# Kernel optimization log

Measured on AMD Instinct MI355X. Metric: run time of the kernel, lower is better.

Reference implementation:

```python
import jax, jax.numpy as jnp
import numpy as np

B, T, D, H, E, K, F = 8, 1024, 512, 8, 8, 2, 2048
HD = D // H
EPS = 1e-5


def _layernorm(x, g, b):
    m = jnp.mean(x, axis=-1, keepdims=True)
    v = jnp.mean((x - m) ** 2, axis=-1, keepdims=True)
    return (x - m) * jax.lax.rsqrt(v + EPS) * g + b


def setup_inputs() -> dict:
    key = jax.random.key(0)
    ks = jax.random.split(key, 12)
    s = lambda d: 1.0 / np.sqrt(d)
    return {
        "x": jax.random.normal(ks[0], (B, T, D), jnp.float32),
        "ln1_g": jnp.ones((D,), jnp.float32),
        "ln1_b": jnp.zeros((D,), jnp.float32),
        "ln2_g": jnp.ones((D,), jnp.float32),
        "ln2_b": jnp.zeros((D,), jnp.float32),
        "Wqkv": jax.random.normal(ks[1], (D, 3 * D), jnp.float32) * s(D),
        "bqkv": jnp.zeros((3 * D,), jnp.float32),
        "Wo": jax.random.normal(ks[2], (D, D), jnp.float32) * s(D),
        "bo": jnp.zeros((D,), jnp.float32),
        "Wg": jax.random.normal(ks[3], (D, E), jnp.float32) * s(D),
        "We1": jax.random.normal(ks[4], (E, D, F), jnp.float32) * s(D),
        "be1": jnp.zeros((E, F), jnp.float32),
        "We2": jax.random.normal(ks[5], (E, F, D), jnp.float32) * s(F),
        "be2": jnp.zeros((E, D), jnp.float32),
    }


def _attn(x, Wqkv, bqkv, Wo, bo):
    qkv = x @ Wqkv + bqkv                      # [B,T,3D]
    q, k, v = jnp.split(qkv, 3, axis=-1)
    q = q.reshape(B, T, H, HD)
    k = k.reshape(B, T, H, HD)
    v = v.reshape(B, T, H, HD)
    scores = jnp.einsum("bqhd,bkhd->bhqk", q, k) / np.sqrt(HD)
    causal = jnp.tril(jnp.ones((T, T), bool))
    scores = jnp.where(causal, scores, jnp.finfo(scores.dtype).min)
    p = jax.nn.softmax(scores, axis=-1)
    o = jnp.einsum("bhqk,bkhd->bqhd", p, v).reshape(B, T, D)
    return o @ Wo + bo


def _moe(h, Wg, We1, be1, We2, be2):
    hf = h.reshape(-1, D)                      # [N,D]
    N = hf.shape[0]
    probs = jax.nn.softmax(hf @ Wg, axis=-1)   # [N,E]
    topw, topi = jax.lax.top_k(probs, K)       # [N,K]
    topw = topw / jnp.sum(topw, axis=-1, keepdims=True)
    gates = jnp.zeros((N, E), hf.dtype).at[jnp.arange(N)[:, None], topi].add(topw)
    out = jnp.zeros_like(hf)
    for e in range(E):                         # fixed small expert loop
        hid = jax.nn.gelu(hf @ We1[e] + be1[e])
        out = out + gates[:, e:e + 1] * (hid @ We2[e] + be2[e])
    return out.reshape(h.shape)


def reference(x, ln1_g, ln1_b, ln2_g, ln2_b, Wqkv, bqkv, Wo, bo, Wg, We1, be1, We2, be2):
    # Pipeline chunking over batch is a scheduling detail; math is the plain block.
    h = x + _attn(_layernorm(x, ln1_g, ln1_b), Wqkv, bqkv, Wo, bo)
    return h + _moe(_layernorm(h, ln2_g, ln2_b), Wg, We1, be1, We2, be2)
```

## Files before the change

### kernel.cpp

```cpp
#include <hip/hip_runtime.h>


typedef unsigned short u16;
typedef unsigned int   u32;
typedef unsigned long long u64;
typedef __attribute__((ext_vector_type(8))) short short8;
typedef __attribute__((ext_vector_type(4))) float f32x4;

#define DEV static __device__ __forceinline__

DEV u16 f2bf(float f){
  union { float f; u32 u; } x; x.f = f;
  return (u16)((x.u + 0x7FFFu + ((x.u >> 16) & 1u)) >> 16);
}
DEV float bf2f(u16 b){
  union { u32 u; float f; } x; x.u = ((u32)b) << 16; return x.f;
}
DEV f32x4 mfma16(short8 a, short8 b, f32x4 c){
  return __builtin_amdgcn_mfma_f32_16x16x32_bf16(a, b, c, 0, 0, 0);
}
DEV void g2l16(const void* g, void* l){
  __builtin_amdgcn_global_load_lds((const __attribute__((address_space(1))) u32*)g,
                                   (__attribute__((address_space(3))) u32*)l, 16, 0, 0);
}
DEV void wait_vm0(){ asm volatile("s_waitcnt vmcnt(0)" ::: "memory"); }

__global__ __launch_bounds__(256) void transpose_cvt2(const float* __restrict__ src,
    u16* __restrict__ dh, u16* __restrict__ dl, int R, int C)
{
  __shared__ float tile[32][33];
  const size_t zb = (size_t)blockIdx.z * R * C;
  src += zb; dh += zb; dl += zb;
  const int tx = threadIdx.x, ty = threadIdx.y;
  const int c0 = blockIdx.x * 32, r0 = blockIdx.y * 32;
  #pragma unroll
  for (int i = 0; i < 4; ++i)
    tile[ty + i*8][tx] = src[(size_t)(r0 + ty + i*8) * C + c0 + tx];
  __syncthreads();
  #pragma unroll
  for (int i = 0; i < 4; ++i){
    float v = tile[tx][ty + i*8];
    size_t o = (size_t)(c0 + ty + i*8) * R + r0 + tx;
    u16 hb = f2bf(v);
    dh[o] = hb;
    dl[o] = f2bf(v - bf2f(hb));
  }
}

__global__ __launch_bounds__(256) void transpose_cvt1(const float* __restrict__ src,
    u16* __restrict__ d, int R, int C)
{
  __shared__ float tile[32][33];
  const size_t zb = (size_t)blockIdx.z * R * C;
  src += zb; d += zb;
  const int tx = threadIdx.x, ty = threadIdx.y;
  const int c0 = blockIdx.x * 32, r0 = blockIdx.y * 32;
  #pragma unroll
  for (int i = 0; i < 4; ++i)
    tile[ty + i*8][tx] = src[(size_t)(r0 + ty + i*8) * C + c0 + tx];
  __syncthreads();
  #pragma unroll
  for (int i = 0; i < 4; ++i)
    d[(size_t)(c0 + ty + i*8) * R + r0 + tx] = f2bf(tile[tx][ty + i*8]);
}

__global__ __launch_bounds__(256) void ln1_kernel(const float* __restrict__ x,
    const float* __restrict__ g, const float* __restrict__ b,
    u16* __restrict__ yh, u16* __restrict__ yl)
{
  const int wid = threadIdx.x >> 6, lane = threadIdx.x & 63;
  const int row = blockIdx.x * 4 + wid;
  const float* xr = x + (size_t)row * 512 + lane * 8;
  f32x4 t0 = ((const f32x4*)xr)[0], t1 = ((const f32x4*)xr)[1];
  float v[8];
  #pragma unroll
  for (int j = 0; j < 8; ++j) v[j] = (j < 4) ? t0[j] : t1[j-4];
  float s = 0.f, q = 0.f;
  #pragma unroll
  for (int j = 0; j < 8; ++j){ s += v[j]; q += v[j]*v[j]; }
  #pragma unroll
  for (int o = 32; o; o >>= 1){ s += __shfl_xor(s, o); q += __shfl_xor(q, o); }
  const float mean = s * (1.f/512.f);
  const float var  = q * (1.f/512.f) - mean*mean;
  const float rstd = rsqrtf(var + 1e-5f);
  f32x4 g0 = ((const f32x4*)(g + lane*8))[0], g1 = ((const f32x4*)(g + lane*8))[1];
  f32x4 b0 = ((const f32x4*)(b + lane*8))[0], b1 = ((const f32x4*)(b + lane*8))[1];
  short8 vh, vl;
  #pragma unroll
  for (int j = 0; j < 8; ++j){
    float gg = (j < 4) ? g0[j] : g1[j-4];
    float bb = (j < 4) ? b0[j] : b1[j-4];
    float y = (v[j]-mean)*rstd*gg + bb;
    u16 hb = f2bf(y);
    vh[j] = (short)hb;
    vl[j] = (short)f2bf(y - bf2f(hb));
  }
  ((short8*)(yh + (size_t)row*512 + lane*8))[0] = vh;
  ((short8*)(yl + (size_t)row*512 + lane*8))[0] = vl;
}

template<int MODE>
__global__ __launch_bounds__(256) void gemm_split2(
    const u16* __restrict__ Ah, const u16* __restrict__ Al,
    const u16* __restrict__ Bh, const u16* __restrict__ Bl,
    const float* __restrict__ bias, int K,
    u16* __restrict__ q_h, u16* __restrict__ q_l, u16* __restrict__ q_m,
    u16* __restrict__ k_h, u16* __restrict__ k_l, u16* __restrict__ k_m,
    u16* __restrict__ v_h, u16* __restrict__ v_l,
    const float* __restrict__ xres, float* __restrict__ hout)
{
  __shared__ u16 Ash[2][128*32], Asl[2][128*32], Bsh[2][128*32], Bsl[2][128*32];
  const int tid = threadIdx.x;
  const int wid = tid >> 6, lane = tid & 63;
  const int wr = wid >> 1, wc = wid & 1;
  const int lr = lane & 15, lg = lane >> 4;
  const int m0 = blockIdx.x * 128, n0 = blockIdx.y * 128;

  size_t aoff[2], boff[2];
  u32 ldso[2];
  #pragma unroll
  for (int r = 0; r < 2; ++r){
    int i = r*256 + tid;
    int row = i >> 2, cc = i & 3;
    int scc = cc ^ ((row >> 1) & 3);
    aoff[r] = ((size_t)(m0+row)*K + scc*8) * 2;
    boff[r] = ((size_t)(n0+row)*K + scc*8) * 2;
    ldso[r] = (u32)(r*256 + wid*64) * 8;
  }

  f32x4 acc[4][4];
  #pragma unroll
  for (int a = 0; a < 4; ++a)
    #pragma unroll
    for (int b = 0; b < 4; ++b) acc[a][b] = 0;

  const char* pAh = (const char*)Ah; const char* pAl = (const char*)Al;
  const char* pBh = (const char*)Bh; const char* pBl = (const char*)Bl;

  auto stage = [&](int sb, int ks){
    const size_t kb = (size_t)ks * 64;
    #pragma unroll
    for (int r = 0; r < 2; ++r){
      g2l16(pAh + aoff[r] + kb, &Ash[sb][0] + ldso[r]);
      g2l16(pAl + aoff[r] + kb, &Asl[sb][0] + ldso[r]);
      g2l16(pBh + boff[r] + kb, &Bsh[sb][0] + ldso[r]);
      g2l16(pBl + boff[r] + kb, &Bsl[sb][0] + ldso[r]);
    }
  };

  const int nks = K >> 5;
  stage(0, 0);
  wait_vm0();
  __syncthreads();
  int buf = 0;
  for (int ks = 0; ks < nks; ++ks){
    if (ks + 1 < nks) stage(buf ^ 1, ks + 1);
    short8 ah[4], al[4], bh[4], bl[4];
    #pragma unroll
    for (int mt = 0; mt < 4; ++mt){
      int row = wr*64 + mt*16 + lr;
      int kcs = lg ^ ((row >> 1) & 3);
      int o = row*32 + kcs*8;
      ah[mt] = *(const short8*)(&Ash[buf][0] + o);
      al[mt] = *(const short8*)(&Asl[buf][0] + o);
    }
    #pragma unroll
    for (int nt = 0; nt < 4; ++nt){
      int row = wc*64 + nt*16 + lr;
      int kcs = lg ^ ((row >> 1) & 3);
      int o = row*32 + kcs*8;
      bh[nt] = *(const short8*)(&Bsh[buf][0] + o);
      bl[nt] = *(const short8*)(&Bsl[buf][0] + o);
    }
    __builtin_amdgcn_s_setprio(1);
    #pragma unroll
    for (int mt = 0; mt < 4; ++mt)
      #pragma unroll
      for (int nt = 0; nt < 4; ++nt){
        f32x4 c = acc[mt][nt];
        c = mfma16(ah[mt], bh[nt], c);
        c = mfma16(ah[mt], bl[nt], c);
        c = mfma16(al[mt], bh[nt], c);
        acc[mt][nt] = c;
      }
    __builtin_amdgcn_s_setprio(0);
    wait_vm0();
    __syncthreads();
    buf ^= 1;
  }

  #pragma unroll
  for (int mt = 0; mt < 4; ++mt){
    #pragma unroll
    for (int nt = 0; nt < 4; ++nt){
      const int col = n0 + wc*64 + nt*16 + lr;
      const float bv = bias[col];
      #pragma unroll
      for (int r2 = 0; r2 < 4; ++r2){
        const int row = m0 + wr*64 + mt*16 + 4*lg + r2;
        const float val = acc[mt][nt][r2] + bv;
        if constexpr (MODE == 0){
          const int which = col >> 9, rem = col & 511;
          const int hh = rem >> 6, hd = rem & 63;
          const int b_ = row >> 10, t_ = row & 1023;
          const size_t idx = ((size_t)(b_*8 + hh)*1024 + t_)*64 + hd;
          const u16 hb = f2bf(val);
          if (which == 2){
            v_h[idx] = hb;
            v_l[idx] = f2bf(val - bf2f(hb));
          } else {
            const float r1 = val - bf2f(hb);
            const u16 lb = f2bf(r1);
            const u16 mb = f2bf(r1 - bf2f(lb));
            if (which == 0){ q_h[idx]=hb; q_l[idx]=lb; q_m[idx]=mb; }
            else           { k_h[idx]=hb; k_l[idx]=lb; k_m[idx]=mb; }
          }
        } else {
          const size_t o = (size_t)row*512 + col;
          hout[o] = val + xres[o];
        }
      }
    }
  }
}

__global__ __launch_bounds__(256) void attn_kernel(
    const u16* __restrict__ q_h, const u16* __restrict__ q_l, const u16* __restrict__ q_m,
    const u16* __restrict__ k_h, const u16* __restrict__ k_l, const u16* __restrict__ k_m,
    const u16* __restrict__ v_h, const u16* __restrict__ v_l,
    u16* __restrict__ aoh, u16* __restrict__ aol)
{
  __shared__ u16 Ksh[64*64], Ksl[64*64], Ksm[64*64];
  __shared__ u16 Vth[64*72], Vtl[64*72];
  __shared__ u16 Ph[4*16*72], Pl[4*16*72];
  const int tid = threadIdx.x, wid = tid >> 6, lane = tid & 63;
  const int lr = lane & 15, lg = lane >> 4;
  const int bfl = blockIdx.x;
  const int xcd = bfl & 7, jj_ = bfl >> 3;
  const int bh = xcd * 8 + (jj_ & 7);
  const int qt = 15 - (jj_ >> 3);
  const int q0 = qt * 64;
  const size_t base = (size_t)bh * 1024 * 64;

  short8 qfh[2], qfl[2], qfm[2];
  {
    const int qrow = q0 + wid*16 + lr;
    #pragma unroll
    for (int c = 0; c < 2; ++c){
      const size_t o = base + (size_t)qrow*64 + c*32 + lg*8;
      qfh[c] = *(const short8*)(q_h + o);
      qfl[c] = *(const short8*)(q_l + o);
      qfm[c] = *(const short8*)(q_m + o);
    }
  }
  f32x4 oacc[4];
  float m_r[4], l_r[4];
  #pragma unroll
  for (int nt = 0; nt < 4; ++nt) oacc[nt] = 0;
  #pragma unroll
  for (int r = 0; r < 4; ++r){ m_r[r] = -1e30f; l_r[r] = 0.f; }

  short8 kreg[3][2];
  short8 vreg[2][2];
  const int pp = tid & 31, d0 = (tid >> 5) * 8;

  auto load_tile = [&](int kt){
    #pragma unroll
    for (int r = 0; r < 2; ++r){
      const int i = r*256 + tid;
      const int row = i >> 3, cc = i & 7;
      const int scc = cc ^ (row & 7);
      const size_t go = base + (size_t)(kt*64 + row)*64 + scc*8;
      kreg[0][r] = *(const short8*)(k_h + go);
      kreg[1][r] = *(const short8*)(k_l + go);
      kreg[2][r] = *(const short8*)(k_m + go);
    }
    const size_t g0 = base + (size_t)(kt*64 + 2*pp)*64 + d0;
    vreg[0][0] = *(const short8*)(v_h + g0);
    vreg[0][1] = *(const short8*)(v_h + g0 + 64);
    vreg[1][0] = *(const short8*)(v_l + g0);
    vreg[1][1] = *(const short8*)(v_l + g0 + 64);
  };

  load_tile(0);
  for (int kt = 0; kt <= qt; ++kt){
    if (kt) __syncthreads();
    #pragma unroll
    for (int r = 0; r < 2; ++r){
      const int o = (r*256 + tid) * 8;
      *(short8*)(Ksh + o) = kreg[0][r];
      *(short8*)(Ksl + o) = kreg[1][r];
      *(short8*)(Ksm + o) = kreg[2][r];
    }
    #pragma unroll
    for (int j = 0; j < 8; ++j){
      u32 ph_ = (u32)(u16)vreg[0][0][j] | ((u32)(u16)vreg[0][1][j] << 16);
      u32 pl_ = (u32)(u16)vreg[1][0][j] | ((u32)(u16)vreg[1][1][j] << 16);
      *(u32*)(Vth + (d0+j)*72 + 2*pp) = ph_;
      *(u32*)(Vtl + (d0+j)*72 + 2*pp) = pl_;
    }
    __syncthreads();
    if (kt < qt) load_tile(kt + 1);
    __builtin_amdgcn_sched_barrier(0);

    f32x4 s[4];
    #pragma unroll
    for (int nt = 0; nt < 4; ++nt) s[nt] = 0;
    __builtin_amdgcn_s_setprio(1);
    #pragma unroll
    for (int c = 0; c < 2; ++c){
      #pragma unroll
      for (int nt = 0; nt < 4; ++nt){
        const int row = nt*16 + lr;
        const int kcs = (c*4 + lg) ^ (row & 7);
        const int o = row*64 + kcs*8;
        short8 kh_ = *(const short8*)(Ksh + o);
        short8 kl_ = *(const short8*)(Ksl + o);
        short8 km_ = *(const short8*)(Ksm + o);
        f32x4 cacc = s[nt];
        cacc = mfma16(qfh[c], kh_, cacc);
        cacc = mfma16(qfh[c], kl_, cacc);
        cacc = mfma16(qfl[c], kh_, cacc);
        cacc = mfma16(qfh[c], km_, cacc);
        cacc = mfma16(qfm[c], kh_, cacc);
        cacc = mfma16(qfl[c], kl_, cacc);
        s[nt] = cacc;
      }
    }
    __builtin_amdgcn_s_setprio(0);
    float sc[4][4];
    const bool last = (kt == qt);
    #pragma unroll
    for (int nt = 0; nt < 4; ++nt)
      #pragma unroll
      for (int r = 0; r < 4; ++r){
        float v = s[nt][r] * 0.125f;
        if (last){
          int qa = q0 + wid*16 + 4*lg + r;
          int ka = kt*64 + nt*16 + lr;
          if (ka > qa) v = -1e30f;
        }
        sc[nt][r] = v;
      }
    float pr[4][4];
    #pragma unroll
    for (int r = 0; r < 4; ++r){
      float mx = fmaxf(fmaxf(sc[0][r], sc[1][r]), fmaxf(sc[2][r], sc[3][r]));
      #pragma unroll
      for (int o2 = 8; o2; o2 >>= 1) mx = fmaxf(mx, __shfl_xor(mx, o2));
      const float nm = fmaxf(m_r[r], mx);
      const float al = __expf(m_r[r] - nm);
      float sum = 0.f;
      #pragma unroll
      for (int nt = 0; nt < 4; ++nt){
        float e_ = __expf(sc[nt][r] - nm);
        pr[nt][r] = e_;
        sum += e_;
      }
      #pragma unroll
      for (int o2 = 8; o2; o2 >>= 1) sum += __shfl_xor(sum, o2);
      l_r[r] = l_r[r]*al + sum;
      m_r[r] = nm;
      #pragma unroll
      for (int nt = 0; nt < 4; ++nt) oacc[nt][r] *= al;
    }
    #pragma unroll
    for (int nt = 0; nt < 4; ++nt)
      #pragma unroll
      for (int r = 0; r < 4; ++r){
        const float pv = pr[nt][r];
        const u16 hb = f2bf(pv);
        const u16 lb = f2bf(pv - bf2f(hb));
        const int o = wid*1152 + (4*lg + r)*72 + nt*16 + lr;
        Ph[o] = hb; Pl[o] = lb;
      }
    #pragma unroll
    for (int c = 0; c < 2; ++c){
      const int po = wid*1152 + lr*72 + c*32 + lg*8;
      short8 pah = *(const short8*)(Ph + po);
      short8 pal = *(const short8*)(Pl + po);
      __builtin_amdgcn_s_setprio(1);
      #pragma unroll
      for (int nt = 0; nt < 4; ++nt){
        const int vo = (nt*16 + lr)*72 + c*32 + lg*8;
        short8 vhf = *(const short8*)(Vth + vo);
        short8 vlf = *(const short8*)(Vtl + vo);
        f32x4 cacc = oacc[nt];
        cacc = mfma16(pah, vhf, cacc);
        cacc = mfma16(pah, vlf, cacc);
        cacc = mfma16(pal, vhf, cacc);
        oacc[nt] = cacc;
      }
      __builtin_amdgcn_s_setprio(0);
    }
  }

  const int b_ = bh >> 3, h_ = bh & 7;
  #pragma unroll
  for (int nt = 0; nt < 4; ++nt)
    #pragma unroll
    for (int r = 0; r < 4; ++r){
      const int qa = q0 + wid*16 + 4*lg + r;
      const float val = oacc[nt][r] / l_r[r];
      const size_t o = ((size_t)(b_*1024 + qa))*512 + h_*64 + nt*16 + lr;
      const u16 hb = f2bf(val);
      aoh[o] = hb;
      aol[o] = f2bf(val - bf2f(hb));
    }
}

__global__ __launch_bounds__(256) void ln2_gate_kernel(const float* __restrict__ h,
    const float* __restrict__ g, const float* __restrict__ b,
    const float* __restrict__ Wg, u16* __restrict__ y2,
    int* __restrict__ ge, float* __restrict__ gw)
{
  const int wid = threadIdx.x >> 6, lane = threadIdx.x & 63;
  const int row = blockIdx.x * 4 + wid;
  const float* xr = h + (size_t)row * 512 + lane * 8;
  f32x4 t0 = ((const f32x4*)xr)[0], t1 = ((const f32x4*)xr)[1];
  float v[8];
  #pragma unroll
  for (int j = 0; j < 8; ++j) v[j] = (j < 4) ? t0[j] : t1[j-4];
  float s = 0.f, q = 0.f;
  #pragma unroll
  for (int j = 0; j < 8; ++j){ s += v[j]; q += v[j]*v[j]; }
  #pragma unroll
  for (int o = 32; o; o >>= 1){ s += __shfl_xor(s, o); q += __shfl_xor(q, o); }
  const float mean = s * (1.f/512.f);
  const float var  = q * (1.f/512.f) - mean*mean;
  const float rstd = rsqrtf(var + 1e-5f);
  f32x4 g0 = ((const f32x4*)(g + lane*8))[0], g1 = ((const f32x4*)(g + lane*8))[1];
  f32x4 b0 = ((const f32x4*)(b + lane*8))[0], b1 = ((const f32x4*)(b + lane*8))[1];
  float yv[8];
  short8 yb;
  #pragma unroll
  for (int j = 0; j < 8; ++j){
    float gg = (j < 4) ? g0[j] : g1[j-4];
    float bb = (j < 4) ? b0[j] : b1[j-4];
    yv[j] = (v[j]-mean)*rstd*gg + bb;
    yb[j] = (short)f2bf(yv[j]);
  }
  ((short8*)(y2 + (size_t)row*512 + lane*8))[0] = yb;

  float lgt[8];
  #pragma unroll
  for (int e = 0; e < 8; ++e) lgt[e] = 0.f;
  #pragma unroll
  for (int j = 0; j < 8; ++j){
    const float* wr_ = Wg + (size_t)(lane*8 + j) * 8;
    #pragma unroll
    for (int e = 0; e < 8; ++e) lgt[e] += yv[j] * wr_[e];
  }
  #pragma unroll
  for (int o = 32; o; o >>= 1){
    #pragma unroll
    for (int e = 0; e < 8; ++e) lgt[e] += __shfl_xor(lgt[e], o);
  }
  if (lane == 0){
    int e0 = 0; float l0 = lgt[0];
    #pragma unroll
    for (int e = 1; e < 8; ++e) if (lgt[e] > l0){ l0 = lgt[e]; e0 = e; }
    int e1 = -1; float l1 = -3e38f;
    #pragma unroll
    for (int e = 0; e < 8; ++e) if (e != e0 && lgt[e] > l1){ l1 = lgt[e]; e1 = e; }
    const float t = expf(l1 - l0);
    const float w0 = 1.f / (1.f + t);
    const float w1 = t * w0;
    ge[row*2]   = e0; ge[row*2+1] = e1;
    gw[row*2]   = w0; gw[row*2+1] = w1;
  }
}

__global__ __launch_bounds__(256) void count_kernel(const int* __restrict__ ge,
                                                    int* __restrict__ cnt)
{
  const int i = blockIdx.x * 256 + threadIdx.x;
  const int lane = threadIdx.x & 63;
  const int e = ge[i];
  #pragma unroll
  for (int ex = 0; ex < 8; ++ex){
    u64 m = __ballot(e == ex);
    if (m && lane == (int)(__ffsll((long long)m) - 1))
      atomicAdd(&cnt[ex], __popcll(m));
  }
}

__global__ void offsets_kernel(int* cnt){
  if (threadIdx.x == 0){
    int o = 0, tp = 0;
    for (int e = 0; e < 8; ++e){
      cnt[8+e] = o; cnt[17+e] = o;
      cnt[25+e] = tp;
      o  += cnt[e];
      tp += (cnt[e] + 127) >> 7;
    }
    cnt[16] = o;
    cnt[33] = tp;
  }
}

__global__ __launch_bounds__(256) void scatter_kernel(const int* __restrict__ ge,
    const float* __restrict__ gw, int* __restrict__ cnt,
    int* __restrict__ rdst, float* __restrict__ rw)
{
  const int i = blockIdx.x * 256 + threadIdx.x;
  const int lane = threadIdx.x & 63;
  const int e = ge[i];
  const float w = gw[i];
  const u64 below = ((u64)1 << lane) - 1;
  int pos = -1;
  #pragma unroll
  for (int ex = 0; ex < 8; ++ex){
    u64 m = __ballot(e == ex);
    if (m){
      const int leader = (int)(__ffsll((long long)m) - 1);
      int base = 0;
      if (lane == leader) base = atomicAdd(&cnt[17 + ex], __popcll(m));
      base = __shfl(base, leader);
      if (e == ex) pos = base + __popcll(m & below);
    }
  }
  rdst[pos] = i;
  rw[pos]   = w;
}

template<int MODE, int TN>
__global__ __launch_bounds__(256, 4) void gemm_moe(
    const u16* __restrict__ A, const u16* __restrict__ Bt,
    const float* __restrict__ bias, int N, int K,
    const int* __restrict__ cntblk,
    const int* __restrict__ rdst, const float* __restrict__ rw,
    u16* __restrict__ hid, float* __restrict__ contrib)
{
  __shared__ u16 As[2][128*32], Bs[2][128*32];
  const int fid = blockIdx.x;
  const int xcd = fid & 7;
  const int j   = fid >> 3;
  const int bpb = 2 * TN;
  const int bi  = j / bpb;
  const int band = bi * 8 + xcd;
  const int r_  = j % bpb;
  const int nt_ = r_ / 2;
  const int mi  = r_ % 2;
  const int mt  = band * 2 + mi;
  if (mt >= cntblk[33]) return;
  int e = 7;
  #pragma unroll
  for (int k = 7; k >= 1; --k) if (mt < cntblk[25 + k]) e = k - 1;
  const int ce = cntblk[e];
  const int eo = cntblk[8 + e];
  const int m0 = (mt - cntblk[25 + e]) * 128;
  const int n0 = nt_ * 128;

  const int tid = threadIdx.x;
  const int wid = tid >> 6, lane = tid & 63;
  const int wr = wid >> 1, wc = wid & 1;
  const int lr = lane & 15, lg = lane >> 4;

  size_t aoff[2], boff[2];
  u32 ldso[2];
  #pragma unroll
  for (int r = 0; r < 2; ++r){
    int i = r*256 + tid;
    int row = i >> 2, cc = i & 3;
    int scc = cc ^ ((row >> 1) & 3);
    int p = eo + m0 + row;
    const int pmax = eo + ce - 1;
    if (p > pmax) p = pmax;
    const int arow = (MODE == 2) ? (rdst[p] >> 1) : p;
    aoff[r] = ((size_t)arow * K + scc*8) * 2;
    boff[r] = (((size_t)e * N + n0 + row) * K + scc*8) * 2;
    ldso[r] = (u32)(r*256 + wid*64) * 8;
  }

  f32x4 acc[4][4];
  #pragma unroll
  for (int a = 0; a < 4; ++a)
    #pragma unroll
    for (int b = 0; b < 4; ++b) acc[a][b] = 0;

  const char* pA = (const char*)A;
  const char* pB = (const char*)Bt;

  auto stage = [&](int sb, int ks){
    const size_t kb = (size_t)ks * 64;
    #pragma unroll
    for (int r = 0; r < 2; ++r){
      g2l16(pA + aoff[r] + kb, &As[sb][0] + ldso[r]);
      g2l16(pB + boff[r] + kb, &Bs[sb][0] + ldso[r]);
    }
  };

  const int nks = K >> 5;
  stage(0, 0);
  wait_vm0();
  __syncthreads();
  int buf = 0;
  for (int ks = 0; ks < nks; ++ks){
    if (ks + 1 < nks) stage(buf ^ 1, ks + 1);
    short8 av[4], bv[4];
    #pragma unroll
    for (int mt2 = 0; mt2 < 4; ++mt2){
      int row = wr*64 + mt2*16 + lr;
      int kcs = lg ^ ((row >> 1) & 3);
      av[mt2] = *(const short8*)(&As[buf][0] + row*32 + kcs*8);
    }
    #pragma unroll
    for (int nt2 = 0; nt2 < 4; ++nt2){
      int row = wc*64 + nt2*16 + lr;
      int kcs = lg ^ ((row >> 1) & 3);
      bv[nt2] = *(const short8*)(&Bs[buf][0] + row*32 + kcs*8);
    }
    __builtin_amdgcn_s_setprio(1);
    #pragma unroll
    for (int mt2 = 0; mt2 < 4; ++mt2)
      #pragma unroll
      for (int nt2 = 0; nt2 < 4; ++nt2)
        acc[mt2][nt2] = mfma16(av[mt2], bv[nt2], acc[mt2][nt2]);
    __builtin_amdgcn_s_setprio(0);
    wait_vm0();
    __syncthreads();
    buf ^= 1;
  }

  const float* bp = bias + (size_t)e * N;
  #pragma unroll
  for (int mt2 = 0; mt2 < 4; ++mt2){
    #pragma unroll
    for (int nt2 = 0; nt2 < 4; ++nt2){
      const int col = n0 + wc*64 + nt2*16 + lr;
      const float bv2 = bp[col];
      #pragma unroll
      for (int r2 = 0; r2 < 4; ++r2){
        const int lrow = wr*64 + mt2*16 + 4*lg + r2;
        if (m0 + lrow < ce){
          const int p = eo + m0 + lrow;
          const float val = acc[mt2][nt2][r2] + bv2;
          if constexpr (MODE == 2){
            const float gx = val;
            const float z2 = 1.5957691216057308f * (gx + 0.044715f*gx*gx*gx);
            const float gl = gx / (1.f + __expf(-z2));
            hid[(size_t)p * N + col] = f2bf(gl);
          } else {
            contrib[(size_t)rdst[p] * 512 + col] = val * rw[p];
          }
        }
      }
    }
  }
}

__global__ __launch_bounds__(256) void final_kernel(const float* __restrict__ h,
    const float* __restrict__ contrib, float* __restrict__ out)
{
  const int i = blockIdx.x * 256 + threadIdx.x;
  const int row = i >> 7, rem = i & 127;
  const f32x4* c4 = (const f32x4*)contrib;
  f32x4 hv = ((const f32x4*)h)[i];
  const size_t b2 = (size_t)(row * 2) * 128 + rem;
  f32x4 a0 = c4[b2];
  f32x4 a1 = c4[b2 + 128];
  ((f32x4*)out)[i] = hv + a0 + a1;
}

extern "C" void kernel_launch(void* const* d_in, const int* in_sizes, int n_in,
                              void* d_out, int out_size, void* d_ws, size_t ws_size,
                              hipStream_t stream)
{
  (void)in_sizes; (void)n_in; (void)out_size; (void)ws_size;
  const float* x    = (const float*)d_in[0];
  const float* ln1g = (const float*)d_in[1];
  const float* ln1b = (const float*)d_in[2];
  const float* ln2g = (const float*)d_in[3];
  const float* ln2b = (const float*)d_in[4];
  const float* Wqkv = (const float*)d_in[5];
  const float* bqkv = (const float*)d_in[6];
  const float* Wo   = (const float*)d_in[7];
  const float* bo   = (const float*)d_in[8];
  const float* Wg   = (const float*)d_in[9];
  const float* We1  = (const float*)d_in[10];
  const float* be1  = (const float*)d_in[11];
  const float* We2  = (const float*)d_in[12];
  const float* be2  = (const float*)d_in[13];
  float* out = (float*)d_out;

  char* ws = (char*)d_ws;
  size_t off_ = 0;
  auto alloc = [&](size_t bytes)->char*{
    char* p = ws + off_;
    off_ = (off_ + bytes + 255) & ~(size_t)255;
    return p;
  };
  u16* wqkvTh = (u16*)alloc((size_t)1536*512*2);
  u16* wqkvTl = (u16*)alloc((size_t)1536*512*2);
  u16* woTh   = (u16*)alloc((size_t)512*512*2);
  u16* woTl   = (u16*)alloc((size_t)512*512*2);
  u16* we1T   = (u16*)alloc((size_t)8*2048*512*2);
  u16* we2T   = (u16*)alloc((size_t)8*512*2048*2);
  u16* y1h    = (u16*)alloc((size_t)8192*512*2);
  u16* y1l    = (u16*)alloc((size_t)8192*512*2);
  u16* qh_    = (u16*)alloc((size_t)8192*64*8*2);
  u16* ql_    = (u16*)alloc((size_t)8192*64*8*2);
  u16* qm_    = (u16*)alloc((size_t)8192*64*8*2);
  u16* kh_    = (u16*)alloc((size_t)8192*64*8*2);
  u16* kl_    = (u16*)alloc((size_t)8192*64*8*2);
  u16* km_    = (u16*)alloc((size_t)8192*64*8*2);
  u16* vh_    = (u16*)alloc((size_t)8192*64*8*2);
  u16* vl_    = (u16*)alloc((size_t)8192*64*8*2);
  u16* aoh    = (u16*)alloc((size_t)8192*512*2);
  u16* aol    = (u16*)alloc((size_t)8192*512*2);
  float* hbuf = (float*)alloc((size_t)8192*512*4);
  u16* y2     = (u16*)alloc((size_t)8192*512*2);
  int* ge     = (int*)alloc((size_t)8192*2*4);
  float* gw   = (float*)alloc((size_t)8192*2*4);
  int* cnt    = (int*)alloc(256);
  int* rdst   = (int*)alloc((size_t)16384*4);
  float* rw   = (float*)alloc((size_t)16384*4);
  u16* hid    = (u16*)alloc((size_t)16384*2048*2);
  float* contrib = (float*)qh_;

  (void)hipMemsetAsync(cnt, 0, 256, stream);

  const dim3 tb(32, 8);
  transpose_cvt2<<<dim3(48, 16, 1), tb, 0, stream>>>(Wqkv, wqkvTh, wqkvTl, 512, 1536);
  transpose_cvt2<<<dim3(16, 16, 1), tb, 0, stream>>>(Wo,   woTh,   woTl,   512, 512);
  transpose_cvt1<<<dim3(64, 16, 8), tb, 0, stream>>>(We1, we1T, 512, 2048);
  transpose_cvt1<<<dim3(16, 64, 8), tb, 0, stream>>>(We2, we2T, 2048, 512);

  ln1_kernel<<<2048, 256, 0, stream>>>(x, ln1g, ln1b, y1h, y1l);

  gemm_split2<0><<<dim3(64, 12), 256, 0, stream>>>(
      y1h, y1l, wqkvTh, wqkvTl, bqkv, 512,
      qh_, ql_, qm_, kh_, kl_, km_, vh_, vl_, nullptr, nullptr);

  attn_kernel<<<dim3(1024), 256, 0, stream>>>(
      qh_, ql_, qm_, kh_, kl_, km_, vh_, vl_, aoh, aol);

  gemm_split2<1><<<dim3(64, 4), 256, 0, stream>>>(
      aoh, aol, woTh, woTl, bo, 512,
      nullptr, nullptr, nullptr, nullptr, nullptr, nullptr, nullptr, nullptr,
      x, hbuf);

  ln2_gate_kernel<<<2048, 256, 0, stream>>>(hbuf, ln2g, ln2b, Wg, y2, ge, gw);
  count_kernel<<<64, 256, 0, stream>>>(ge, cnt);
  offsets_kernel<<<1, 64, 0, stream>>>(cnt);
  scatter_kernel<<<64, 256, 0, stream>>>(ge, gw, cnt, rdst, rw);

  gemm_moe<2, 16><<<dim3(2304), 256, 0, stream>>>(
      y2, we1T, be1, 2048, 512, cnt, rdst, rw, hid, nullptr);
  gemm_moe<3, 4><<<dim3(576), 256, 0, stream>>>(
      hid, we2T, be2, 512, 2048, cnt, rdst, rw, nullptr, contrib);

  final_kernel<<<4096, 256, 0, stream>>>(hbuf, contrib, out);
}
```

Before: 422.5 us.

## Use 256x256 tiles with 512 threads for the first MoE expert GEMM

Replaces the first expert GEMM (up-projection plus GELU) with a new kernel using 256x256 output tiles, 64-wide K steps, 8 waves per block and double-buffered direct global-to-LDS loads with XOR swizzle. The offsets kernel now also computes per-expert prefix counts of 256-row tiles to index the larger tiles. The goal is more data reuse per loaded byte and fewer blocks. In exchange it uses much more LDS per block and lower occupancy, and wastes more padding rows per expert.

```diff
diff --git a/kernel.cpp b/kernel.cpp
--- a/kernel.cpp
+++ b/kernel.cpp
@@ -24,6 +24,7 @@
                                    (__attribute__((address_space(3))) u32*)l, 16, 0, 0);
 }
 DEV void wait_vm0(){ asm volatile("s_waitcnt vmcnt(0)" ::: "memory"); }
+DEV void wait_vm8(){ asm volatile("s_waitcnt vmcnt(8)" ::: "memory"); }
 
 __global__ __launch_bounds__(256) void transpose_cvt2(const float* __restrict__ src,
     u16* __restrict__ dh, u16* __restrict__ dl, int R, int C)
@@ -487,15 +488,18 @@
 
 __global__ void offsets_kernel(int* cnt){
   if (threadIdx.x == 0){
-    int o = 0, tp = 0;
+    int o = 0, tp = 0, tp2 = 0;
     for (int e = 0; e < 8; ++e){
       cnt[8+e] = o; cnt[17+e] = o;
       cnt[25+e] = tp;
-      o  += cnt[e];
-      tp += (cnt[e] + 127) >> 7;
+      cnt[34+e] = tp2;
+      o   += cnt[e];
+      tp  += (cnt[e] + 127) >> 7;
+      tp2 += (cnt[e] + 255) >> 8;
     }
     cnt[16] = o;
     cnt[33] = tp;
+    cnt[42] = tp2;
   }
 }
 
@@ -522,6 +526,127 @@
   }
   rdst[pos] = i;
   rw[pos]   = w;
+}
+
+__global__ __launch_bounds__(512, 2) void gemm_moe2_256(
+    const u16* __restrict__ A, const u16* __restrict__ Bt,
+    const float* __restrict__ bias,
+    const int* __restrict__ cntblk,
+    const int* __restrict__ rdst,
+    u16* __restrict__ hid)
+{
+  __shared__ u16 As[2][256*64], Bs[2][256*64];
+  const int fid = blockIdx.x;
+  const int xcd = fid & 7;
+  const int j   = fid >> 3;
+  const int bi  = j >> 3;
+  const int nt_ = j & 7;
+  const int mt  = bi * 8 + xcd;
+  if (mt >= cntblk[42]) return;
+  int e = 7;
+  #pragma unroll
+  for (int k = 7; k >= 1; --k) if (mt < cntblk[34 + k]) e = k - 1;
+  const int ce = cntblk[e];
+  const int eo = cntblk[8 + e];
+  const int m0 = (mt - cntblk[34 + e]) * 256;
+  const int n0 = nt_ * 256;
+
+  const int tid = threadIdx.x;
+  const int wid = tid >> 6, lane = tid & 63;
+  const int wr = wid >> 2, wc = wid & 3;
+  const int lr = lane & 15, lg = lane >> 4;
+
+  size_t aoff[4], boff[4];
+  u32 ldso[4];
+  #pragma unroll
+  for (int r = 0; r < 4; ++r){
+    const int i = r*512 + tid;
+    const int row = i >> 3, cc = i & 7;
+    const int scc = cc ^ (row & 7);
+    int p = eo + m0 + row;
+    const int pmax = eo + ce - 1;
+    if (p > pmax) p = pmax;
+    const int arow = rdst[p] >> 1;
+    aoff[r] = ((size_t)arow * 512 + scc*8) * 2;
+    boff[r] = (((size_t)e * 2048 + n0 + row) * 512 + scc*8) * 2;
+    ldso[r] = (u32)i * 8;
+  }
+
+  f32x4 acc[8][4];
+  #pragma unroll
+  for (int a = 0; a < 8; ++a)
+    #pragma unroll
+    for (int b = 0; b < 4; ++b) acc[a][b] = 0;
+
+  const char* pA = (const char*)A;
+  const char* pB = (const char*)Bt;
+
+  auto stage = [&](int sb, int kt){
+    const size_t kb = (size_t)kt * 128;
+    #pragma unroll
+    for (int r = 0; r < 4; ++r){
+      g2l16(pA + aoff[r] + kb, &As[sb][0] + ldso[r]);
+      g2l16(pB + boff[r] + kb, &Bs[sb][0] + ldso[r]);
+    }
+  };
+
+  auto compute = [&](int buf){
+    #pragma unroll
+    for (int ks2 = 0; ks2 < 2; ++ks2){
+      short8 av[8], bv[4];
+      #pragma unroll
+      for (int mt2 = 0; mt2 < 8; ++mt2){
+        const int row = wr*128 + mt2*16 + lr;
+        const int ch = (ks2*4 + lg) ^ (row & 7);
+        av[mt2] = *(const short8*)(&As[buf][0] + row*64 + ch*8);
+      }
+      #pragma unroll
+      for (int nt2 = 0; nt2 < 4; ++nt2){
+        const int row = wc*64 + nt2*16 + lr;
+        const int ch = (ks2*4 + lg) ^ (row & 7);
+        bv[nt2] = *(const short8*)(&Bs[buf][0] + row*64 + ch*8);
+      }
+      __builtin_amdgcn_s_setprio(1);
+      #pragma unroll
+      for (int mt2 = 0; mt2 < 8; ++mt2)
+        #pragma unroll
+        for (int nt2 = 0; nt2 < 4; ++nt2)
+          acc[mt2][nt2] = mfma16(av[mt2], bv[nt2], acc[mt2][nt2]);
+      __builtin_amdgcn_s_setprio(0);
+    }
+  };
+
+  stage(0, 0);
+  int buf = 0;
+  for (int kt = 0; kt < 8; ++kt){
+    if (kt + 1 < 8){ stage(buf ^ 1, kt + 1); wait_vm8(); }
+    else           { wait_vm0(); }
+    __syncthreads();
+    compute(buf);
+    __syncthreads();
+    buf ^= 1;
+  }
+
+  const float* bp = bias + (size_t)e * 2048;
+  #pragma unroll
+  for (int mt2 = 0; mt2 < 8; ++mt2){
+    #pragma unroll
+    for (int nt2 = 0; nt2 < 4; ++nt2){
+      const int col = n0 + wc*64 + nt2*16 + lr;
+      const float bv2 = bp[col];
+      #pragma unroll
+      for (int r2 = 0; r2 < 4; ++r2){
+        const int lrow = wr*128 + mt2*16 + 4*lg + r2;
+        if (m0 + lrow < ce){
+          const int p = eo + m0 + lrow;
+          const float gx = acc[mt2][nt2][r2] + bv2;
+          const float z2 = 1.5957691216057308f * (gx + 0.044715f*gx*gx*gx);
+          const float gl = gx / (1.f + __expf(-z2));
+          hid[(size_t)p * 2048 + col] = f2bf(gl);
+        }
+      }
+    }
+  }
 }
 
 template<int MODE, int TN>
@@ -746,8 +871,8 @@
   offsets_kernel<<<1, 64, 0, stream>>>(cnt);
   scatter_kernel<<<64, 256, 0, stream>>>(ge, gw, cnt, rdst, rw);
 
-  gemm_moe<2, 16><<<dim3(2304), 256, 0, stream>>>(
-      y2, we1T, be1, 2048, 512, cnt, rdst, rw, hid, nullptr);
+  gemm_moe2_256<<<dim3(576), 512, 0, stream>>>(
+      y2, we1T, be1, cnt, rdst, hid);
   gemm_moe<3, 4><<<dim3(576), 256, 0, stream>>>(
       hid, we2T, be2, 512, 2048, cnt, rdst, rw, nullptr, contrib);
 
```

Measured after the change: 449.0 us. 6.3% more time.
